# Kernel tuning notes

Measured on AMD Instinct MI355X. Metric: run time of the kernel, lower is better.

## Reference

```python
import jax, jax.numpy as jnp
import numpy as np

IN_F, OUT_F, LAT, RES, K, B = 512, 512, 512, 64, 3, 8
EPS = 1e-08
C_LIN = 1.0 / np.sqrt(LAT)          # EqualizedWeight scale for linear
C_CONV = 1.0 / np.sqrt(IN_F * K * K)  # EqualizedWeight scale for conv


def setup_inputs() -> dict:
    key = jax.random.key(0)
    k1, k2, k3, k4 = jax.random.split(key, 4)
    return {
        "x": jax.random.normal(k1, (B, IN_F, RES, RES), dtype=jnp.float32),
        "latent": jax.random.normal(k2, (B, LAT), dtype=jnp.float32),
        "w_lin": jax.random.normal(k3, (IN_F, LAT), dtype=jnp.float32),
        "b_lin": jnp.ones((IN_F,), dtype=jnp.float32),
        "w_conv": jax.random.normal(k4, (OUT_F, IN_F, K, K), dtype=jnp.float32),
        "b_conv": jnp.zeros((OUT_F,), dtype=jnp.float32),
    }


def reference(x, latent, w_lin, b_lin, w_conv, b_conv):
    # EqualizedLinear: s = latent @ (w_lin*c).T + b_lin*lr_mul  -> [B, IN_F]
    s = latent @ (w_lin * C_LIN).T + b_lin
    # ModulatedConv2d. Per-sample weight w[b,o,i,k,k] = (w_conv*c)[o,i,k,k]*s[b,i],
    # demodulated by sigma_inv[b,o] = rsqrt(sum_{i,k,k} w^2 + eps).
    w = w_conv * C_CONV  # [O, I, K, K]
    # sum_{k,k} w^2 over spatial -> [O, I], then contract with s^2 -> [B, O]
    w2 = jnp.sum(w * w, axis=(2, 3))  # [O, I]
    sigma_inv = jax.lax.rsqrt(jnp.einsum('oi,bi->bo', w2, s * s) + EPS)
    # conv(x, w*s_b) == conv(x * s_b, w): modulate input, single batched conv,
    # then demodulate output per (b, o). Avoids materializing B*O filters.
    x_mod = x * s[:, :, None, None]
    y = jax.lax.conv_general_dilated(
        x_mod, w,
        window_strides=(1, 1),
        padding=[((K - 1) // 2, (K - 1) // 2)] * 2,
        dimension_numbers=('NCHW', 'OIHW', 'NCHW'),
    )
    y = y * sigma_inv[:, :, None, None] + b_conv[None, :, None, None]
    return y
```

## Files before the change

### kernel.cpp

```cpp
#include <hip/hip_runtime.h>
#include <hip/hip_bf16.h>

#define IN_F 512
#define OUT_F 512
#define LATD 512
#define RES 64
#define BATCH 8
#define EPSV 1e-8f

static constexpr float C_LIN  = 0.04419417382415922f;
static constexpr float C_CONV = 0.014731391274719739f;

typedef __attribute__((ext_vector_type(8)))  short short8;
typedef __attribute__((ext_vector_type(16))) float f32x16;

union BF { __hip_bfloat16 h; short s; };

__device__ __forceinline__ void async_load16(const char* g, char* l) {
  __builtin_amdgcn_global_load_lds(
      (const __attribute__((address_space(1))) unsigned int*)g,
      (__attribute__((address_space(3))) unsigned int*)l, 16, 0, 0);
}

__global__ void k_compute_s(const float* __restrict__ latent,
                            const float* __restrict__ w_lin,
                            const float* __restrict__ b_lin,
                            float* __restrict__ s) {
  const int i = blockIdx.x;
  const int lane = threadIdx.x;
  const float4* wl = (const float4*)(w_lin + (size_t)i * LATD);
  const float4 w0 = wl[lane * 2], w1 = wl[lane * 2 + 1];
  float acc[BATCH];
#pragma unroll
  for (int b = 0; b < BATCH; ++b) {
    const float4* lt = (const float4*)(latent + (size_t)b * LATD);
    const float4 l0 = lt[lane * 2], l1 = lt[lane * 2 + 1];
    acc[b] = w0.x * l0.x + w0.y * l0.y + w0.z * l0.z + w0.w * l0.w +
             w1.x * l1.x + w1.y * l1.y + w1.z * l1.z + w1.w * l1.w;
  }
#pragma unroll
  for (int b = 0; b < BATCH; ++b) {
    float v = acc[b];
#pragma unroll
    for (int off = 32; off > 0; off >>= 1) v += __shfl_down(v, off);
    if (lane == 0) s[b * IN_F + i] = v * C_LIN + b_lin[i];
  }
}

__global__ void k_prep_w(const float* __restrict__ w_conv,
                         short* __restrict__ wb,
                         float* __restrict__ w2,
                         char* __restrict__ xmp) {
  const int t = blockIdx.x * 256 + threadIdx.x;
  const int o = t >> 9;
  const int i = t & 511;
  const float* src = w_conv + (size_t)t * 9;
  const int c = i >> 4, hf0 = (i >> 3) & 1, ch = i & 7;
  const int ob = o >> 7, ol = o & 127;
  short* dst = wb + (size_t)(c * 4 + ob) * 18432 + hf0 * 1024 + ol * 8 + ch;
  float sum = 0.f;
#pragma unroll
  for (int tap = 0; tap < 9; ++tap) {
    const float v = src[tap] * C_CONV;
    sum += v * v;
    BF cv; cv.h = __float2bfloat16(v);
    dst[tap * 2048] = cv.s;
  }
  w2[t] = sum;

  if (blockIdx.x < 256) {
    char* base = xmp + (size_t)blockIdx.x * 139392;
    for (int q = threadIdx.x; q < 520; q += 256) {
      int h, hf, w;
      if (q < 132)      { h = 0;  hf = (q >= 66) ? 1 : 0; w = q - hf * 66; }
      else if (q < 264) { const int r = q - 132; h = 65; hf = (r >= 66) ? 1 : 0; w = r - hf * 66; }
      else              { const int r = q - 264; h = (r >> 2) + 1; hf = (r >> 1) & 1; w = (r & 1) * 65; }
      *(uint4*)(base + ((size_t)(h * 132 + hf * 66 + w)) * 16) = make_uint4(0u, 0u, 0u, 0u);
    }
  }
}

__global__ void k_sigma(const float* __restrict__ w2,
                        const float* __restrict__ s,
                        float* __restrict__ sigma_inv) {
  const int o = blockIdx.x * 4 + (threadIdx.x >> 6);
  const int lane = threadIdx.x & 63;
  float acc[BATCH];
#pragma unroll
  for (int b = 0; b < BATCH; ++b) acc[b] = 0.f;
#pragma unroll
  for (int k = 0; k < 8; ++k) {
    const int i = k * 64 + lane;
    const float w = w2[o * IN_F + i];
#pragma unroll
    for (int b = 0; b < BATCH; ++b) {
      const float sv = s[b * IN_F + i];
      acc[b] += w * sv * sv;
    }
  }
#pragma unroll
  for (int b = 0; b < BATCH; ++b) {
    float v = acc[b];
#pragma unroll
    for (int off = 32; off > 0; off >>= 1) v += __shfl_down(v, off);
    if (lane == 0) sigma_inv[b * OUT_F + o] = rsqrtf(v + EPSV);
  }
}

__global__ void k_modulate(const float* __restrict__ x,
                           const float* __restrict__ s,
                           char* __restrict__ xmp) {
  const int h    = blockIdx.x & 63;
  const int ic32 = (blockIdx.x >> 6) & 15;
  const int b    = blockIdx.x >> 10;
  __shared__ float tile[32][65];
  const int tid = threadIdx.x;
  {
    const int il = tid >> 3, w8 = (tid & 7) * 8;
    const int i = ic32 * 32 + il;
    const float sv = s[b * IN_F + i];
    const float* xp = x + (((size_t)(b * IN_F + i) * RES + h) * RES + w8);
    const float4 v0 = *(const float4*)xp;
    const float4 v1 = *(const float4*)(xp + 4);
    tile[il][w8 + 0] = v0.x * sv; tile[il][w8 + 1] = v0.y * sv;
    tile[il][w8 + 2] = v0.z * sv; tile[il][w8 + 3] = v0.w * sv;
    tile[il][w8 + 4] = v1.x * sv; tile[il][w8 + 5] = v1.y * sv;
    tile[il][w8 + 6] = v1.z * sv; tile[il][w8 + 7] = v1.w * sv;
  }
  __syncthreads();
  {
    const int w = tid >> 2, part = tid & 3;
    const int chalf = part >> 1, hf = part & 1;
    short8 pk;
#pragma unroll
    for (int j = 0; j < 8; ++j) {
      BF cv; cv.h = __float2bfloat16(tile[chalf * 16 + hf * 8 + j][w]);
      pk[j] = cv.s;
    }
    const int c = ic32 * 2 + chalf;
    char* dst = xmp + (size_t)(c * 8 + b) * 139392 +
                ((size_t)(h + 1) * 132 + hf * 66 + (w + 1)) * 16;
    *(short8*)dst = pk;
  }
}

__global__ __launch_bounds__(512, 2)
void k_conv(const char* __restrict__ xmp,
            const short* __restrict__ wbg,
            const float* __restrict__ sigma_inv,
            const float* __restrict__ b_conv,
            float* __restrict__ out) {
  __shared__ __align__(16) char lds[115968];
  const int l = blockIdx.x;
  const int ob = (l >> 3) & 3;
  const int b  = l & 7;
  const int h0 = (l >> 5) * 8;
  const int o0 = ob * 128;
  const int tid = threadIdx.x;
  const int wave = tid >> 6, lane = tid & 63;
  const int l31 = lane & 31, half = lane >> 5;
  const int oh = wave >> 2;
  const int q  = wave & 3;
  const int r0 = (q >> 1) * 4;
  const int c0 = (q & 1) * 32;

  f32x16 acc[2][4];
#pragma unroll
  for (int i = 0; i < 2; ++i)
#pragma unroll
    for (int j = 0; j < 4; ++j)
#pragma unroll
      for (int r = 0; r < 16; ++r) acc[i][j][r] = 0.f;

  const char* xsrc0 = xmp + (size_t)b * 139392 + (size_t)h0 * 2112;
  const char* wsrc0 = (const char*)wbg + (size_t)ob * 36864;

#pragma unroll
  for (int k = 0; k < 2; ++k) {
    const int j = tid + k * 512;
    async_load16(xsrc0 + j * 16, lds + j * 16);
  }
  if (tid < 296) { const int j = 1024 + tid; async_load16(xsrc0 + j * 16, lds + j * 16); }
#pragma unroll
  for (int k = 0; k < 4; ++k) {
    const int j = tid + k * 512;
    async_load16(wsrc0 + j * 16, lds + 42240 + j * 16);
  }
  if (tid < 256) { const int j = 2048 + tid; async_load16(wsrc0 + j * 16, lds + 42240 + j * 16); }
  __syncthreads();

  for (int ic = 0; ic < 32; ++ic) {
    const int p = ic & 1;
    if (ic + 1 < 32) {
      const char* xs  = xsrc0 + (size_t)(ic + 1) * (8 * 139392);
      const char* wsr = wsrc0 + (size_t)(ic + 1) * 147456;
      char* xd = lds + (p ^ 1) * 21120;
      char* wd = lds + 42240 + (p ^ 1) * 36864;
#pragma unroll
      for (int k = 0; k < 2; ++k) {
        const int j = tid + k * 512;
        async_load16(xs + j * 16, xd + j * 16);
      }
      if (tid < 296) { const int j = 1024 + tid; async_load16(xs + j * 16, xd + j * 16); }
#pragma unroll
      for (int k = 0; k < 4; ++k) {
        const int j = tid + k * 512;
        async_load16(wsr + j * 16, wd + j * 16);
      }
      if (tid < 256) { const int j = 2048 + tid; async_load16(wsr + j * 16, wd + j * 16); }
    }
    const char* xp = lds + p * 21120;
    const char* wp = lds + 42240 + p * 36864;
#pragma unroll
    for (int dw = 0; dw < 3; ++dw) {
      short8 brow[6];
#pragma unroll
      for (int rr = 0; rr < 6; ++rr)
        brow[rr] = *(const short8*)(
            xp + (((r0 + rr) * 132) + half * 66 + c0 + dw + l31) * 16);
#pragma unroll
      for (int dh = 0; dh < 3; ++dh) {
        const int tap = dh * 3 + dw;
        short8 a[2];
#pragma unroll
        for (int f = 0; f < 2; ++f)
          a[f] = *(const short8*)(
              wp + tap * 4096 + half * 2048 + (oh * 64 + f * 32 + l31) * 16);
#pragma unroll
        for (int tpr = 0; tpr < 4; ++tpr)
#pragma unroll
          for (int f = 0; f < 2; ++f)
            acc[f][tpr] = __builtin_amdgcn_mfma_f32_32x32x16_bf16(
                a[f], brow[tpr + dh], acc[f][tpr], 0, 0, 0);
      }
    }
    __syncthreads();
  }

#pragma unroll
  for (int f = 0; f < 2; ++f) {
#pragma unroll
    for (int g = 0; g < 4; ++g) {
#pragma unroll
      for (int r = 0; r < 4; ++r) {
        const int o = o0 + oh * 64 + f * 32 + r + 8 * g + 4 * half;
        const float sig  = sigma_inv[b * OUT_F + o];
        const float bias = b_conv[o];
        const int reg = g * 4 + r;
#pragma unroll
        for (int tpr = 0; tpr < 4; ++tpr) {
          const int h = h0 + r0 + tpr;
          const int w = c0 + l31;
          out[(((size_t)(b * OUT_F + o) * RES + h) * RES) + w] =
              acc[f][tpr][reg] * sig + bias;
        }
      }
    }
  }
}

extern "C" void kernel_launch(void* const* d_in, const int* in_sizes, int n_in,
                              void* d_out, int out_size, void* d_ws, size_t ws_size,
                              hipStream_t stream) {
  const float* x      = (const float*)d_in[0];
  const float* latent = (const float*)d_in[1];
  const float* w_lin  = (const float*)d_in[2];
  const float* b_lin  = (const float*)d_in[3];
  const float* w_conv = (const float*)d_in[4];
  const float* b_conv = (const float*)d_in[5];
  float* out = (float*)d_out;

  char* ws = (char*)d_ws;
  char*  xmp       = ws;
  short* wb        = (short*)(ws + 35684352);
  float* w2        = (float*)(ws + 40402944);
  float* s         = (float*)(ws + 41451520);
  float* sigma_inv = (float*)(ws + 41467904);

  k_compute_s<<<IN_F, 64, 0, stream>>>(latent, w_lin, b_lin, s);
  k_prep_w<<<1024, 256, 0, stream>>>(w_conv, wb, w2, xmp);
  k_sigma<<<128, 256, 0, stream>>>(w2, s, sigma_inv);
  k_modulate<<<BATCH * 16 * RES, 256, 0, stream>>>(x, s, xmp);
  k_conv<<<256, 512, 0, stream>>>(xmp, wb, sigma_inv, b_conv, out);
}
```

Baseline: 258.2 us.

## Merge prep kernels into two launches and raise MFMA wave priority

Folds the style-vector computation into the weight-prep kernel and the sigma computation into the modulation kernel, cutting five launches to three so fewer launch gaps and tail-drain periods sit between dependent stages. The sigma blocks run as extra blocks alongside the modulation grid, which is safe because sigma only needs w2 and s from the previous launch. It also wraps the MFMA inner loop of the conv kernel in s_setprio so waves issuing matrix ops get scheduling priority over waves issuing loads. The fused kernels carry larger register and LDS footprints across all blocks, which may reduce occupancy for the simpler paths.

```diff
diff --git a/kernel.cpp b/kernel.cpp
--- a/kernel.cpp
+++ b/kernel.cpp
@@ -22,51 +22,32 @@
       (__attribute__((address_space(3))) unsigned int*)l, 16, 0, 0);
 }
 
-__global__ void k_compute_s(const float* __restrict__ latent,
-                            const float* __restrict__ w_lin,
-                            const float* __restrict__ b_lin,
-                            float* __restrict__ s) {
-  const int i = blockIdx.x;
-  const int lane = threadIdx.x;
-  const float4* wl = (const float4*)(w_lin + (size_t)i * LATD);
-  const float4 w0 = wl[lane * 2], w1 = wl[lane * 2 + 1];
-  float acc[BATCH];
-#pragma unroll
-  for (int b = 0; b < BATCH; ++b) {
-    const float4* lt = (const float4*)(latent + (size_t)b * LATD);
-    const float4 l0 = lt[lane * 2], l1 = lt[lane * 2 + 1];
-    acc[b] = w0.x * l0.x + w0.y * l0.y + w0.z * l0.z + w0.w * l0.w +
-             w1.x * l1.x + w1.y * l1.y + w1.z * l1.z + w1.w * l1.w;
-  }
-#pragma unroll
-  for (int b = 0; b < BATCH; ++b) {
-    float v = acc[b];
-#pragma unroll
-    for (int off = 32; off > 0; off >>= 1) v += __shfl_down(v, off);
-    if (lane == 0) s[b * IN_F + i] = v * C_LIN + b_lin[i];
-  }
-}
-
-__global__ void k_prep_w(const float* __restrict__ w_conv,
-                         short* __restrict__ wb,
-                         float* __restrict__ w2,
-                         char* __restrict__ xmp) {
+__global__ void k_prep(const float* __restrict__ w_conv,
+                       short* __restrict__ wb,
+                       float* __restrict__ w2,
+                       char* __restrict__ xmp,
+                       const float* __restrict__ latent,
+                       const float* __restrict__ w_lin,
+                       const float* __restrict__ b_lin,
+                       float* __restrict__ s) {
   const int t = blockIdx.x * 256 + threadIdx.x;
-  const int o = t >> 9;
-  const int i = t & 511;
-  const float* src = w_conv + (size_t)t * 9;
-  const int c = i >> 4, hf0 = (i >> 3) & 1, ch = i & 7;
-  const int ob = o >> 7, ol = o & 127;
-  short* dst = wb + (size_t)(c * 4 + ob) * 18432 + hf0 * 1024 + ol * 8 + ch;
-  float sum = 0.f;
-#pragma unroll
-  for (int tap = 0; tap < 9; ++tap) {
-    const float v = src[tap] * C_CONV;
-    sum += v * v;
-    BF cv; cv.h = __float2bfloat16(v);
-    dst[tap * 2048] = cv.s;
-  }
-  w2[t] = sum;
+  {
+    const int o = t >> 9;
+    const int i = t & 511;
+    const float* src = w_conv + (size_t)t * 9;
+    const int c = i >> 4, hf0 = (i >> 3) & 1, ch = i & 7;
+    const int ob = o >> 7, ol = o & 127;
+    short* dst = wb + (size_t)(c * 4 + ob) * 18432 + hf0 * 1024 + ol * 8 + ch;
+    float sum = 0.f;
+#pragma unroll
+    for (int tap = 0; tap < 9; ++tap) {
+      const float v = src[tap] * C_CONV;
+      sum += v * v;
+      BF cv; cv.h = __float2bfloat16(v);
+      dst[tap * 2048] = cv.s;
+    }
+    w2[t] = sum;
+  }
 
   if (blockIdx.x < 256) {
     char* base = xmp + (size_t)blockIdx.x * 139392;
@@ -78,41 +59,64 @@
       *(uint4*)(base + ((size_t)(h * 132 + hf * 66 + w)) * 16) = make_uint4(0u, 0u, 0u, 0u);
     }
   }
-}
-
-__global__ void k_sigma(const float* __restrict__ w2,
-                        const float* __restrict__ s,
-                        float* __restrict__ sigma_inv) {
-  const int o = blockIdx.x * 4 + (threadIdx.x >> 6);
-  const int lane = threadIdx.x & 63;
-  float acc[BATCH];
-#pragma unroll
-  for (int b = 0; b < BATCH; ++b) acc[b] = 0.f;
-#pragma unroll
-  for (int k = 0; k < 8; ++k) {
-    const int i = k * 64 + lane;
-    const float w = w2[o * IN_F + i];
+
+  if (blockIdx.x < 128) {
+    const int wv = threadIdx.x >> 6, lane = threadIdx.x & 63;
+    const int i = blockIdx.x * 4 + wv;
+    const float4* wl = (const float4*)(w_lin + (size_t)i * LATD);
+    const float4 w0 = wl[lane * 2], w1 = wl[lane * 2 + 1];
+    float acc[BATCH];
 #pragma unroll
     for (int b = 0; b < BATCH; ++b) {
-      const float sv = s[b * IN_F + i];
-      acc[b] += w * sv * sv;
-    }
-  }
-#pragma unroll
-  for (int b = 0; b < BATCH; ++b) {
-    float v = acc[b];
-#pragma unroll
-    for (int off = 32; off > 0; off >>= 1) v += __shfl_down(v, off);
-    if (lane == 0) sigma_inv[b * OUT_F + o] = rsqrtf(v + EPSV);
-  }
-}
-
-__global__ void k_modulate(const float* __restrict__ x,
-                           const float* __restrict__ s,
-                           char* __restrict__ xmp) {
-  const int h    = blockIdx.x & 63;
-  const int ic32 = (blockIdx.x >> 6) & 15;
-  const int b    = blockIdx.x >> 10;
+      const float4* lt = (const float4*)(latent + (size_t)b * LATD);
+      const float4 l0 = lt[lane * 2], l1 = lt[lane * 2 + 1];
+      acc[b] = w0.x * l0.x + w0.y * l0.y + w0.z * l0.z + w0.w * l0.w +
+               w1.x * l1.x + w1.y * l1.y + w1.z * l1.z + w1.w * l1.w;
+    }
+#pragma unroll
+    for (int b = 0; b < BATCH; ++b) {
+      float v = acc[b];
+#pragma unroll
+      for (int off = 32; off > 0; off >>= 1) v += __shfl_down(v, off);
+      if (lane == 0) s[b * IN_F + i] = v * C_LIN + b_lin[i];
+    }
+  }
+}
+
+__global__ void k_mod_sigma(const float* __restrict__ x,
+                            const float* __restrict__ s,
+                            char* __restrict__ xmp,
+                            const float* __restrict__ w2,
+                            float* __restrict__ sigma_inv) {
+  if (blockIdx.x < 128) {
+    const int o = blockIdx.x * 4 + (threadIdx.x >> 6);
+    const int lane = threadIdx.x & 63;
+    float acc[BATCH];
+#pragma unroll
+    for (int b = 0; b < BATCH; ++b) acc[b] = 0.f;
+#pragma unroll
+    for (int k = 0; k < 8; ++k) {
+      const int i = k * 64 + lane;
+      const float w = w2[o * IN_F + i];
+#pragma unroll
+      for (int b = 0; b < BATCH; ++b) {
+        const float sv = s[b * IN_F + i];
+        acc[b] += w * sv * sv;
+      }
+    }
+#pragma unroll
+    for (int b = 0; b < BATCH; ++b) {
+      float v = acc[b];
+#pragma unroll
+      for (int off = 32; off > 0; off >>= 1) v += __shfl_down(v, off);
+      if (lane == 0) sigma_inv[b * OUT_F + o] = rsqrtf(v + EPSV);
+    }
+    return;
+  }
+  const int bid  = blockIdx.x - 128;
+  const int h    = bid & 63;
+  const int ic32 = (bid >> 6) & 15;
+  const int b    = bid >> 10;
   __shared__ float tile[32][65];
   const int tid = threadIdx.x;
   {
@@ -226,12 +230,14 @@
         for (int f = 0; f < 2; ++f)
           a[f] = *(const short8*)(
               wp + tap * 4096 + half * 2048 + (oh * 64 + f * 32 + l31) * 16);
+        __builtin_amdgcn_s_setprio(1);
 #pragma unroll
         for (int tpr = 0; tpr < 4; ++tpr)
 #pragma unroll
           for (int f = 0; f < 2; ++f)
             acc[f][tpr] = __builtin_amdgcn_mfma_f32_32x32x16_bf16(
                 a[f], brow[tpr + dh], acc[f][tpr], 0, 0, 0);
+        __builtin_amdgcn_s_setprio(0);
       }
     }
     __syncthreads();
@@ -277,9 +283,7 @@
   float* s         = (float*)(ws + 41451520);
   float* sigma_inv = (float*)(ws + 41467904);
 
-  k_compute_s<<<IN_F, 64, 0, stream>>>(latent, w_lin, b_lin, s);
-  k_prep_w<<<1024, 256, 0, stream>>>(w_conv, wb, w2, xmp);
-  k_sigma<<<128, 256, 0, stream>>>(w2, s, sigma_inv);
-  k_modulate<<<BATCH * 16 * RES, 256, 0, stream>>>(x, s, xmp);
+  k_prep<<<1024, 256, 0, stream>>>(w_conv, wb, w2, xmp, latent, w_lin, b_lin, s);
+  k_mod_sigma<<<128 + BATCH * 16 * RES, 256, 0, stream>>>(x, s, xmp, w2, sigma_inv);
   k_conv<<<256, 512, 0, stream>>>(xmp, wb, sigma_inv, b_conv, out);
 }
```

After: 249.0 us. -3.6%, faster.
